# Optimization experiments

Hardware: AMD Instinct MI355X
Metric: run time of the kernel (lower is better)

The kernel has to match this reference:

```python
import jax, jax.numpy as jnp
import numpy as np
from jax import lax

CLIP = 10.0


def setup_inputs() -> dict:
    key = jax.random.key(0)
    k1, k2, k3, k4 = jax.random.split(key, 4)
    B, T, I, H = 64, 512, 512, 512
    x = jax.random.normal(k1, (B, T, I), dtype=jnp.float32)
    kernel = jax.random.normal(k2, (I, H), dtype=jnp.float32) * 0.05
    recurrent_kernel = jax.random.normal(k3, (H, H), dtype=jnp.float32) * 0.05
    bias_i = jax.random.normal(k4, (H,), dtype=jnp.float32) * 0.05
    h0 = jnp.zeros((B, H), dtype=jnp.float32)
    return {"x": x, "kernel": kernel, "recurrent_kernel": recurrent_kernel,
            "bias_i": bias_i, "h0": h0}


def reference(x, kernel, recurrent_kernel, bias_i, h0):
    # Elman RNN: Ht = tanh(clip(Xt@W + Ht-1@R + b, -clip, clip))
    def step(h, xt):
        g = xt @ kernel + h @ recurrent_kernel + bias_i  # [B, H]
        h_new = jnp.tanh(jnp.clip(g, -CLIP, CLIP))
        return h_new, h_new

    xs = jnp.swapaxes(x, 0, 1)  # [T, B, I] for scan over time
    h_last, ys = lax.scan(step, h0, xs)
    outputs = jnp.swapaxes(ys, 0, 1)  # [B, T, H]
    return outputs, h_last
```

## Files before the change

### kernel.cpp

```cpp
#include <hip/hip_runtime.h>

#define Bdim 64
#define Tdim 512
#define Idim 512
#define Hdim 512
#define CLIPV 10.0f
#define NREGG 50
#define NLDSG 14

typedef __attribute__((ext_vector_type(4))) float f32x4;
typedef __attribute__((ext_vector_type(8))) short bf16x8;
typedef _Float16 half2v __attribute__((ext_vector_type(2)));
typedef __fp16 fp16x2 __attribute__((ext_vector_type(2)));

__device__ __forceinline__ ushort f2bf(float f) {
    unsigned u = __builtin_bit_cast(unsigned, f);
    u += 0x7fffu + ((u >> 16) & 1u);
    return (ushort)(u >> 16);
}
__device__ __forceinline__ float bf2f(ushort h) {
    return __builtin_bit_cast(float, (unsigned)h << 16);
}
__device__ __forceinline__ void split_bf(float f, ushort& h, ushort& l) {
    h = f2bf(f);
    l = f2bf(f - bf2f(h));
}
__device__ __forceinline__ float dot2acc(uint r, uint h2, float acc) {
#if __has_builtin(__builtin_amdgcn_fdot2)
    return __builtin_amdgcn_fdot2(__builtin_bit_cast(half2v, r),
                                  __builtin_bit_cast(half2v, h2), acc, false);
#else
    half2v a = __builtin_bit_cast(half2v, r);
    half2v b = __builtin_bit_cast(half2v, h2);
    return acc + (float)a.x * (float)b.x + (float)a.y * (float)b.y;
#endif
}
__device__ __forceinline__ uint packf16(float a, float b) {
    _Float16 fa = (_Float16)a, fb = (_Float16)b;
    return (uint)__builtin_bit_cast(ushort, fa) |
           ((uint)__builtin_bit_cast(ushort, fb) << 16);
}
__device__ __forceinline__ uint pkrtz(float a, float b) {
#if __has_builtin(__builtin_amdgcn_cvt_pkrtz)
    fp16x2 p = __builtin_amdgcn_cvt_pkrtz(a, b);
    return __builtin_bit_cast(uint, p);
#else
    return packf16(a, b);
#endif
}
__device__ __forceinline__ float fastrcp(float x) {
#if __has_builtin(__builtin_amdgcn_rcpf)
    return __builtin_amdgcn_rcpf(x);
#else
    return 1.0f / x;
#endif
}

__global__ __launch_bounds__(256) void transpose_w_kernel(const float* __restrict__ w,
                                                          ushort* __restrict__ wth,
                                                          ushort* __restrict__ wtl) {
    int idx = blockIdx.x * 256 + threadIdx.x;
    int k = idx >> 9, n = idx & 511;
    ushort h, l;
    split_bf(w[idx], h, l);
    wth[n * Idim + k] = h;
    wtl[n * Idim + k] = l;
}

__global__ __launch_bounds__(256) void pack_r_kernel(const float* __restrict__ Rw,
                                                     uint* __restrict__ rpk) {
    int d = blockIdx.x * 256 + threadIdx.x;
    int g = d >> 11;
    int rem = d & 2047;
    int t = rem >> 2, r = rem & 3;
    int j = g >> 1, half = g & 1;
    int w = t >> 6, l = t & 63;
    int kp = w * 32 + j;
    int c  = half * 256 + l * 4 + r;
    rpk[d] = packf16(Rw[(size_t)(2 * kp) * Hdim + c],
                     Rw[(size_t)(2 * kp + 1) * Hdim + c]);
}

#define BM 128
#define BN 128
#define BK 32
__global__ __launch_bounds__(256) void gemm_xw(
    const float* __restrict__ A,
    const ushort* __restrict__ Bth,
    const ushort* __restrict__ Btl,
    const float* __restrict__ bias,
    float* __restrict__ C,
    int M, int N, int K)
{
    __shared__ ushort AsH[BM][BK];
    __shared__ ushort AsL[BM][BK];
    __shared__ ushort BsH[BN][BK];
    __shared__ ushort BsL[BN][BK];
    int bm = blockIdx.x, bn = blockIdx.y;
    int tid = threadIdx.x;
    int wave = tid >> 6, lane = tid & 63;
    int wr = wave >> 1, wc = wave & 1;
    f32x4 acc[4][4] = {};
    const int row0 = bm * BM, col0 = bn * BN;
    const int sr = tid >> 1;
    const int sc = (tid & 1) * 16;

    for (int kt = 0; kt < K; kt += BK) {
        const float* gA = A + (size_t)(row0 + sr) * K + kt + sc;
        #pragma unroll
        for (int q = 0; q < 4; ++q) {
            float4 v = *(const float4*)(gA + q * 4);
            ushort4 h4, l4;
            split_bf(v.x, h4.x, l4.x);
            split_bf(v.y, h4.y, l4.y);
            split_bf(v.z, h4.z, l4.z);
            split_bf(v.w, h4.w, l4.w);
            *(ushort4*)&AsH[sr][sc + q * 4] = h4;
            *(ushort4*)&AsL[sr][sc + q * 4] = l4;
        }
        const int4* gBh = (const int4*)(Bth + (size_t)(col0 + sr) * K + kt + sc);
        *(int4*)&BsH[sr][sc]     = gBh[0];
        *(int4*)&BsH[sr][sc + 8] = gBh[1];
        const int4* gBl = (const int4*)(Btl + (size_t)(col0 + sr) * K + kt + sc);
        *(int4*)&BsL[sr][sc]     = gBl[0];
        *(int4*)&BsL[sr][sc + 8] = gBl[1];
        __syncthreads();

        const int r = lane & 15, kg = lane >> 4;
        bf16x8 ah[4], al[4], bh[4], bl[4];
        #pragma unroll
        for (int m = 0; m < 4; ++m) {
            ah[m] = *(const bf16x8*)&AsH[wr * 64 + m * 16 + r][kg * 8];
            al[m] = *(const bf16x8*)&AsL[wr * 64 + m * 16 + r][kg * 8];
        }
        #pragma unroll
        for (int n = 0; n < 4; ++n) {
            bh[n] = *(const bf16x8*)&BsH[wc * 64 + n * 16 + r][kg * 8];
            bl[n] = *(const bf16x8*)&BsL[wc * 64 + n * 16 + r][kg * 8];
        }
        #pragma unroll
        for (int m = 0; m < 4; ++m)
            #pragma unroll
            for (int n = 0; n < 4; ++n) {
                acc[m][n] = __builtin_amdgcn_mfma_f32_16x16x32_bf16(ah[m], bh[n], acc[m][n], 0, 0, 0);
                acc[m][n] = __builtin_amdgcn_mfma_f32_16x16x32_bf16(ah[m], bl[n], acc[m][n], 0, 0, 0);
                acc[m][n] = __builtin_amdgcn_mfma_f32_16x16x32_bf16(al[m], bh[n], acc[m][n], 0, 0, 0);
            }
        __syncthreads();
    }

    const int cl = lane & 15, rg = lane >> 4;
    #pragma unroll
    for (int n = 0; n < 4; ++n) {
        int gc = col0 + wc * 64 + n * 16 + cl;
        float bv = bias[gc];
        #pragma unroll
        for (int m = 0; m < 4; ++m) {
            int gr = row0 + wr * 64 + m * 16 + rg * 4;
            #pragma unroll
            for (int r2 = 0; r2 < 4; ++r2)
                C[(size_t)(gr + r2) * N + gc] = acc[m][n][r2] + bv;
        }
    }
}

__global__ __launch_bounds__(512, 2) void rnn_reg_kernel(
    const uint* __restrict__ Rpk,
    float* __restrict__ out,
    float* __restrict__ hlast,
    const float* __restrict__ h0)
{
    __shared__ uint Rlds[NLDSG * 2048];
    __shared__ float part[2][8][Hdim];

    const int tid = threadIdx.x;
    const int row = blockIdx.x;
    const int w   = tid >> 6;
    const int l   = tid & 63;
    const int li  = l & 31;
    const int fcol = w * 64 + 2 * li;

    uint4 rr4[NREGG];
    const uint* rbase = Rpk + tid * 4;
    #pragma unroll
    for (int i = 0; i < NREGG; ++i)
        rr4[i] = *(const uint4*)(rbase + i * 2048);
    #pragma unroll
    for (int g = 0; g < NLDSG; ++g)
        *(uint4*)&Rlds[g * 2048 + tid * 4] =
            *(const uint4*)(rbase + (NREGG + g) * 2048);

    uint hval = packf16(h0[row * Hdim + fcol], h0[row * Hdim + fcol + 1]);
    __syncthreads();

    float* orow = out + (size_t)row * Tdim * Hdim;
    float2 pre = *(const float2*)(orow + fcol);

    for (int t = 0; t < Tdim; ++t, orow += Hdim) {
        float2 pre_nxt = *(const float2*)(orow + Hdim + fcol);

        float a0 = 0.f, a1 = 0.f, a2 = 0.f, a3 = 0.f;
        float a4 = 0.f, a5 = 0.f, a6 = 0.f, a7 = 0.f;
        #pragma unroll
        for (int j = 0; j < NREGG / 2; ++j) {
            uint hvi = __builtin_amdgcn_readlane(hval, j);
            uint4 rA = rr4[2 * j], rB = rr4[2 * j + 1];
            a0 = dot2acc(rA.x, hvi, a0);
            a1 = dot2acc(rA.y, hvi, a1);
            a2 = dot2acc(rA.z, hvi, a2);
            a3 = dot2acc(rA.w, hvi, a3);
            a4 = dot2acc(rB.x, hvi, a4);
            a5 = dot2acc(rB.y, hvi, a5);
            a6 = dot2acc(rB.z, hvi, a6);
            a7 = dot2acc(rB.w, hvi, a7);
        }
        #pragma unroll
        for (int j = 0; j < NLDSG / 2; ++j) {
            uint hvi = __builtin_amdgcn_readlane(hval, NREGG / 2 + j);
            uint4 rA = *(const uint4*)&Rlds[(2 * j) * 2048 + tid * 4];
            uint4 rB = *(const uint4*)&Rlds[(2 * j + 1) * 2048 + tid * 4];
            a0 = dot2acc(rA.x, hvi, a0);
            a1 = dot2acc(rA.y, hvi, a1);
            a2 = dot2acc(rA.z, hvi, a2);
            a3 = dot2acc(rA.w, hvi, a3);
            a4 = dot2acc(rB.x, hvi, a4);
            a5 = dot2acc(rB.y, hvi, a5);
            a6 = dot2acc(rB.z, hvi, a6);
            a7 = dot2acc(rB.w, hvi, a7);
        }
        const int p = t & 1;
        *(f32x4*)&part[p][w][l * 4]       = (f32x4){a0, a1, a2, a3};
        *(f32x4*)&part[p][w][256 + l * 4] = (f32x4){a4, a5, a6, a7};
        __syncthreads();

        float s0 = pre.x, s1 = pre.y;
        #pragma unroll
        for (int e = 0; e < 8; ++e) {
            float2 pp = *(const float2*)&part[p][e][fcol];
            s0 += pp.x; s1 += pp.y;
        }
        s0 = fminf(fmaxf(s0, -CLIPV), CLIPV);
        s1 = fminf(fmaxf(s1, -CLIPV), CLIPV);
        float e0 = __expf(2.0f * s0), e1 = __expf(2.0f * s1);
        float v0 = (e0 - 1.0f) * fastrcp(e0 + 1.0f);
        float v1 = (e1 - 1.0f) * fastrcp(e1 + 1.0f);
        hval = pkrtz(v0, v1);
        if (l < 32) {
            *(float2*)(orow + fcol) = make_float2(v0, v1);
            if (t == Tdim - 1)
                *(float2*)&hlast[row * Hdim + fcol] = make_float2(v0, v1);
        }
        pre = pre_nxt;
    }
}

extern "C" void kernel_launch(void* const* d_in, const int* in_sizes, int n_in,
                              void* d_out, int out_size, void* d_ws, size_t ws_size,
                              hipStream_t stream) {
    const float* x    = (const float*)d_in[0];
    const float* W    = (const float*)d_in[1];
    const float* R    = (const float*)d_in[2];
    const float* bias = (const float*)d_in[3];
    const float* h0   = (const float*)d_in[4];
    float* out = (float*)d_out;

    ushort* wth = (ushort*)d_ws;
    ushort* wtl = wth + (size_t)Idim * Hdim;
    uint* rpk   = (uint*)((char*)d_ws + (1u << 20));

    transpose_w_kernel<<<(Idim * Hdim + 255) / 256, 256, 0, stream>>>(W, wth, wtl);
    pack_r_kernel<<<512, 256, 0, stream>>>(R, rpk);

    dim3 gg(Bdim * Tdim / BM, Hdim / BN);
    gemm_xw<<<gg, 256, 0, stream>>>(x, wth, wtl, bias, out, Bdim * Tdim, Hdim, Idim);

    rnn_reg_kernel<<<Bdim, 512, 0, stream>>>(
        rpk, out, out + (size_t)Bdim * Tdim * Hdim, h0);
}
```

Before: 844.6 us.

## Split RNN recurrence across 1024 threads with the recurrent matrix fully in registers

The recurrent kernel grows from 512 to 1024 threads per batch row. Each of the 16 waves now owns a 32-row slice of K, so the whole packed recurrent matrix fits in registers (32 uint4 per thread), and the LDS-resident part of the weights is removed. This halves the serial dot-product chain per timestep and drops the LDS weight reads. In exchange the cross-wave partial-sum reduction doubles to 16 terms, and the tighter register budget (128 VGPRs per thread at this occupancy) risks spilling.

```diff
diff --git a/kernel.cpp b/kernel.cpp
--- a/kernel.cpp
+++ b/kernel.cpp
@@ -5,8 +5,6 @@
 #define Idim 512
 #define Hdim 512
 #define CLIPV 10.0f
-#define NREGG 50
-#define NLDSG 14
 
 typedef __attribute__((ext_vector_type(4))) float f32x4;
 typedef __attribute__((ext_vector_type(8))) short bf16x8;
@@ -70,12 +68,12 @@
 __global__ __launch_bounds__(256) void pack_r_kernel(const float* __restrict__ Rw,
                                                      uint* __restrict__ rpk) {
     int d = blockIdx.x * 256 + threadIdx.x;
-    int g = d >> 11;
-    int rem = d & 2047;
+    int g = d >> 12;
+    int rem = d & 4095;
     int t = rem >> 2, r = rem & 3;
     int j = g >> 1, half = g & 1;
     int w = t >> 6, l = t & 63;
-    int kp = w * 32 + j;
+    int kp = w * 16 + j;
     int c  = half * 256 + l * 4 + r;
     rpk[d] = packf16(Rw[(size_t)(2 * kp) * Hdim + c],
                      Rw[(size_t)(2 * kp + 1) * Hdim + c]);
@@ -164,34 +162,28 @@
     }
 }
 
-__global__ __launch_bounds__(512, 2) void rnn_reg_kernel(
+__global__ __launch_bounds__(1024, 4) void rnn_reg_kernel(
     const uint* __restrict__ Rpk,
     float* __restrict__ out,
     float* __restrict__ hlast,
     const float* __restrict__ h0)
 {
-    __shared__ uint Rlds[NLDSG * 2048];
-    __shared__ float part[2][8][Hdim];
+    __shared__ float part[2][16][Hdim];
 
     const int tid = threadIdx.x;
     const int row = blockIdx.x;
     const int w   = tid >> 6;
     const int l   = tid & 63;
-    const int li  = l & 31;
-    const int fcol = w * 64 + 2 * li;
-
-    uint4 rr4[NREGG];
+    const int li  = l & 15;
+    const int fcol = w * 32 + 2 * li;
+
+    uint4 rr4[32];
     const uint* rbase = Rpk + tid * 4;
     #pragma unroll
-    for (int i = 0; i < NREGG; ++i)
-        rr4[i] = *(const uint4*)(rbase + i * 2048);
-    #pragma unroll
-    for (int g = 0; g < NLDSG; ++g)
-        *(uint4*)&Rlds[g * 2048 + tid * 4] =
-            *(const uint4*)(rbase + (NREGG + g) * 2048);
+    for (int i = 0; i < 32; ++i)
+        rr4[i] = *(const uint4*)(rbase + i * 4096);
 
     uint hval = packf16(h0[row * Hdim + fcol], h0[row * Hdim + fcol + 1]);
-    __syncthreads();
 
     float* orow = out + (size_t)row * Tdim * Hdim;
     float2 pre = *(const float2*)(orow + fcol);
@@ -202,9 +194,10 @@
         float a0 = 0.f, a1 = 0.f, a2 = 0.f, a3 = 0.f;
         float a4 = 0.f, a5 = 0.f, a6 = 0.f, a7 = 0.f;
         #pragma unroll
-        for (int j = 0; j < NREGG / 2; ++j) {
+        for (int j = 0; j < 16; ++j) {
             uint hvi = __builtin_amdgcn_readlane(hval, j);
-            uint4 rA = rr4[2 * j], rB = rr4[2 * j + 1];
+            uint4 rA = rr4[2 * j];
+            uint4 rB = rr4[2 * j + 1];
             a0 = dot2acc(rA.x, hvi, a0);
             a1 = dot2acc(rA.y, hvi, a1);
             a2 = dot2acc(rA.z, hvi, a2);
@@ -214,20 +207,6 @@
             a6 = dot2acc(rB.z, hvi, a6);
             a7 = dot2acc(rB.w, hvi, a7);
         }
-        #pragma unroll
-        for (int j = 0; j < NLDSG / 2; ++j) {
-            uint hvi = __builtin_amdgcn_readlane(hval, NREGG / 2 + j);
-            uint4 rA = *(const uint4*)&Rlds[(2 * j) * 2048 + tid * 4];
-            uint4 rB = *(const uint4*)&Rlds[(2 * j + 1) * 2048 + tid * 4];
-            a0 = dot2acc(rA.x, hvi, a0);
-            a1 = dot2acc(rA.y, hvi, a1);
-            a2 = dot2acc(rA.z, hvi, a2);
-            a3 = dot2acc(rA.w, hvi, a3);
-            a4 = dot2acc(rB.x, hvi, a4);
-            a5 = dot2acc(rB.y, hvi, a5);
-            a6 = dot2acc(rB.z, hvi, a6);
-            a7 = dot2acc(rB.w, hvi, a7);
-        }
         const int p = t & 1;
         *(f32x4*)&part[p][w][l * 4]       = (f32x4){a0, a1, a2, a3};
         *(f32x4*)&part[p][w][256 + l * 4] = (f32x4){a4, a5, a6, a7};
@@ -235,7 +214,7 @@
 
         float s0 = pre.x, s1 = pre.y;
         #pragma unroll
-        for (int e = 0; e < 8; ++e) {
+        for (int e = 0; e < 16; ++e) {
             float2 pp = *(const float2*)&part[p][e][fcol];
             s0 += pp.x; s1 += pp.y;
         }
@@ -245,7 +224,7 @@
         float v0 = (e0 - 1.0f) * fastrcp(e0 + 1.0f);
         float v1 = (e1 - 1.0f) * fastrcp(e1 + 1.0f);
         hval = pkrtz(v0, v1);
-        if (l < 32) {
+        if (l < 16) {
             *(float2*)(orow + fcol) = make_float2(v0, v1);
             if (t == Tdim - 1)
                 *(float2*)&hlast[row * Hdim + fcol] = make_float2(v0, v1);
@@ -274,6 +253,6 @@
     dim3 gg(Bdim * Tdim / BM, Hdim / BN);
     gemm_xw<<<gg, 256, 0, stream>>>(x, wth, wtl, bias, out, Bdim * Tdim, Hdim, Idim);
 
-    rnn_reg_kernel<<<Bdim, 512, 0, stream>>>(
+    rnn_reg_kernel<<<Bdim, 1024, 0, stream>>>(
         rpk, out, out + (size_t)Bdim * Tdim * Hdim, h0);
 }
```

New measurement: 1.583 ms. 1.87x slower.
